# Kernel tuning notes

Hardware: AMD Instinct MI355X
Metric: run time of the kernel (lower is better)

Reference implementation:

```python
import jax, jax.numpy as jnp
import numpy as np

DIM = 1024
NUM_HEADS = 16
HEAD_DIM = DIM // NUM_HEADS
SCALE = HEAD_DIM ** -0.5


def setup_inputs() -> dict:
    key = jax.random.key(0)
    ks = jax.random.split(key, 6)
    B, N, C = 2, 2048, DIM
    std = C ** -0.5
    return {
        "x_t": jax.random.normal(ks[0], (B, N, C), dtype=jnp.float32),
        "x_s": jax.random.normal(ks[1], (B, N, C), dtype=jnp.float32),
        "W_q": jax.random.normal(ks[2], (C, C), dtype=jnp.float32) * std,
        "W_kv": jax.random.normal(ks[3], (C, 2 * C), dtype=jnp.float32) * std,
        "W_fuse": jax.random.normal(ks[4], (C, C), dtype=jnp.float32) * std,
        "b_fuse": jax.random.normal(ks[5], (C,), dtype=jnp.float32) * 0.01,
    }


def reference(x_t, x_s, W_q, W_kv, W_fuse, b_fuse):
    B, N, C = x_t.shape
    H, D = NUM_HEADS, HEAD_DIM
    # q projection (no bias, qkv_bias=False): [B,N,C] -> [B,H,N,D]
    q = (x_t @ W_q).reshape(B, N, H, D).transpose(0, 2, 1, 3)
    # kv projection: [B,N,2C] -> k,v each [B,H,N,D]
    kv = (x_s @ W_kv).reshape(B, N, 2, H, D).transpose(2, 0, 3, 1, 4)
    k, v = kv[0], kv[1]
    # attention scores [B,H,N,N]
    attn = jnp.einsum("bhnd,bhmd->bhnm", q, k) * SCALE
    attn = jax.nn.softmax(attn, axis=-1)
    # weighted values -> [B,N,C]
    a = jnp.einsum("bhnm,bhmd->bhnd", attn, v).transpose(0, 2, 1, 3).reshape(B, N, C)
    # fuse projection (with bias); dropouts are identity (p=0)
    return a @ W_fuse + b_fuse
```

## Files before the change

kernel.cpp:

```cpp
#include <hip/hip_runtime.h>

#define SEQ 2048

typedef short short8 __attribute__((ext_vector_type(8)));
typedef float floatx4 __attribute__((ext_vector_type(4)));

static __device__ __forceinline__ unsigned short f2bf(float f) {
    unsigned int u = __builtin_bit_cast(unsigned int, f);
    u = (u + 0x7fffu + ((u >> 16) & 1u)) >> 16;
    return (unsigned short)u;
}

#if __has_builtin(__builtin_amdgcn_cvt_pk_bf16_f32)
typedef __bf16 bf16x2 __attribute__((ext_vector_type(2)));
static __device__ __forceinline__ unsigned int pk_bf16(float a, float b) {
    bf16x2 v = __builtin_amdgcn_cvt_pk_bf16_f32(a, b);
    return __builtin_bit_cast(unsigned int, v);
}
#else
static __device__ __forceinline__ unsigned int pk_bf16(float a, float b) {
    return (unsigned int)f2bf(a) | ((unsigned int)f2bf(b) << 16);
}
#endif

#define GLD16(gp, lp)                                                        \
    __builtin_amdgcn_global_load_lds(                                        \
        (const __attribute__((address_space(1))) unsigned int*)(gp),         \
        (__attribute__((address_space(3))) unsigned int*)(lp), 16, 0, 0)

#define SWZ(row, col) ((col) ^ (((row) & 7) << 3))

__global__ void cvt2_kernel(const float4* __restrict__ a, const float4* __restrict__ b,
                            ushort4* __restrict__ oa, ushort4* __restrict__ ob, float sa) {
    int i = blockIdx.x * blockDim.x + threadIdx.x;
    if (i < 1048576) {
        float4 v = a[i];
        ushort4 o;
        o.x = f2bf(v.x * sa); o.y = f2bf(v.y * sa);
        o.z = f2bf(v.z * sa); o.w = f2bf(v.w * sa);
        oa[i] = o;
    } else {
        int j = i - 1048576;
        float4 v = b[j];
        ushort4 o;
        o.x = f2bf(v.x); o.y = f2bf(v.y);
        o.z = f2bf(v.z); o.w = f2bf(v.w);
        ob[j] = o;
    }
}

__global__ void transpose_all(const float* __restrict__ Wq, const float* __restrict__ Wkv,
                              const float* __restrict__ Wf,
                              unsigned short* __restrict__ oq, unsigned short* __restrict__ okv,
                              unsigned short* __restrict__ of_) {
    __shared__ float tile[32][33];
    int bx = blockIdx.x;
    const float* in; unsigned short* out; int N, t;
    if (bx < 1024)      { in = Wq;  out = oq;  N = 1024; t = bx; }
    else if (bx < 3072) { in = Wkv; out = okv; N = 2048; t = bx - 1024; }
    else                { in = Wf;  out = of_; N = 1024; t = bx - 3072; }
    int nb = N >> 5;
    int n0 = (t % nb) * 32, k0 = (t / nb) * 32;
    int tx = threadIdx.x, ty = threadIdx.y;
#pragma unroll
    for (int i = 0; i < 4; i++)
        tile[ty + i * 8][tx] = in[(size_t)(k0 + ty + i * 8) * N + n0 + tx];
    __syncthreads();
#pragma unroll
    for (int i = 0; i < 4; i++)
        out[(size_t)(n0 + ty + i * 8) * 1024 + k0 + tx] = f2bf(tile[tx][ty + i * 8]);
}

__global__ __launch_bounds__(256, 3)
void gemm_qkv(const unsigned short* __restrict__ xt,
              const unsigned short* __restrict__ xs,
              const unsigned short* __restrict__ wq,
              const unsigned short* __restrict__ wkv,
              unsigned short* __restrict__ q_ws,
              unsigned short* __restrict__ k_ws,
              unsigned short* __restrict__ vt_ws) {
    __shared__ unsigned short sA[128][64];
    __shared__ unsigned short sB[128][64];
    int tid = threadIdx.x, wave = tid >> 6, lane = tid & 63;
    int l15 = lane & 15, quad = lane >> 4;
    int cx = blockIdx.x;
    bool isq = cx < 8;
    const unsigned short* A  = isq ? xt : xs;
    const unsigned short* Bt = isq ? wq : wkv;
    int C0 = (isq ? cx : cx - 8) * 128;
    int R0 = blockIdx.y * 128;
    int wr = (wave >> 1) * 64, wc = (wave & 1) * 64;
    int srow = lane >> 3, scol = (lane & 7) * 8;

    floatx4 acc[4][4];
#pragma unroll
    for (int i = 0; i < 4; i++)
#pragma unroll
        for (int j = 0; j < 4; j++) acc[i][j] = (floatx4){0.f, 0.f, 0.f, 0.f};

    for (int kt = 0; kt < 16; kt++) {
        __syncthreads();
#pragma unroll
        for (int c = 0; c < 4; c++) {
            int rb = wave * 32 + c * 8;
            GLD16(&A [(size_t)(R0 + rb + srow) * 1024 + kt * 64 + scol], &sA[rb][0]);
            GLD16(&Bt[(size_t)(C0 + rb + srow) * 1024 + kt * 64 + scol], &sB[rb][0]);
        }
        __syncthreads();
#pragma unroll
        for (int ks = 0; ks < 2; ks++) {
            short8 af[4], bf[4];
#pragma unroll
            for (int mt = 0; mt < 4; mt++)
                af[mt] = *(const short8*)&sA[wr + mt * 16 + l15][ks * 32 + quad * 8];
#pragma unroll
            for (int nt = 0; nt < 4; nt++)
                bf[nt] = *(const short8*)&sB[wc + nt * 16 + l15][ks * 32 + quad * 8];
#pragma unroll
            for (int mt = 0; mt < 4; mt++)
#pragma unroll
                for (int nt = 0; nt < 4; nt++)
                    acc[mt][nt] = __builtin_amdgcn_mfma_f32_16x16x32_bf16(af[mt], bf[nt], acc[mt][nt], 0, 0, 0);
        }
    }

    int b = R0 >> 11, nb0 = (R0 & 2047) + wr;
#pragma unroll
    for (int mt = 0; mt < 4; mt++) {
#pragma unroll
        for (int nt = 0; nt < 4; nt++) {
            int col = C0 + wc + nt * 16 + l15;
            if (isq) {
                int h = col >> 6, d = col & 63;
#pragma unroll
                for (int r = 0; r < 4; r++) {
                    int n = nb0 + mt * 16 + quad * 4 + r;
                    q_ws[((size_t)((b * 16 + h) * 2048 + n)) * 64 + d] = f2bf(acc[mt][nt][r]);
                }
            } else if (col < 1024) {
                int h = col >> 6, d = col & 63;
#pragma unroll
                for (int r = 0; r < 4; r++) {
                    int n = nb0 + mt * 16 + quad * 4 + r;
                    k_ws[((size_t)((b * 16 + h) * 2048 + n)) * 64 + d] = f2bf(acc[mt][nt][r]);
                }
            } else {
                int cc = col - 1024, h = cc >> 6, d = cc & 63;
                int n = nb0 + mt * 16 + quad * 4;
                ushort4 pk;
                pk.x = f2bf(acc[mt][nt][0]); pk.y = f2bf(acc[mt][nt][1]);
                pk.z = f2bf(acc[mt][nt][2]); pk.w = f2bf(acc[mt][nt][3]);
                *(ushort4*)&vt_ws[((size_t)((b * 16 + h) * 64 + d)) * 2048 + n] = pk;
            }
        }
    }
}

__global__ __launch_bounds__(256, 3)
void gemm_fuse(const unsigned short* __restrict__ A,
               const unsigned short* __restrict__ Bt,
               float* __restrict__ out, const float* __restrict__ bias) {
    __shared__ unsigned short sA[128][64];
    __shared__ unsigned short sB[64][64];
    int tid = threadIdx.x, wave = tid >> 6, lane = tid & 63;
    int l15 = lane & 15, quad = lane >> 4;
    int R0 = blockIdx.y * 128, C0 = blockIdx.x * 64;
    int wr = (wave >> 1) * 64, wc = (wave & 1) * 32;
    int srow = lane >> 3, scol = (lane & 7) * 8;

    floatx4 acc[4][2];
#pragma unroll
    for (int i = 0; i < 4; i++)
#pragma unroll
        for (int j = 0; j < 2; j++) acc[i][j] = (floatx4){0.f, 0.f, 0.f, 0.f};

    for (int kt = 0; kt < 16; kt++) {
        __syncthreads();
#pragma unroll
        for (int c = 0; c < 4; c++) {
            int rb = wave * 32 + c * 8;
            GLD16(&A[(size_t)(R0 + rb + srow) * 1024 + kt * 64 + scol], &sA[rb][0]);
        }
#pragma unroll
        for (int c = 0; c < 2; c++) {
            int rb = wave * 16 + c * 8;
            GLD16(&Bt[(size_t)(C0 + rb + srow) * 1024 + kt * 64 + scol], &sB[rb][0]);
        }
        __syncthreads();
#pragma unroll
        for (int ks = 0; ks < 2; ks++) {
            short8 af[4], bf[2];
#pragma unroll
            for (int mt = 0; mt < 4; mt++)
                af[mt] = *(const short8*)&sA[wr + mt * 16 + l15][ks * 32 + quad * 8];
#pragma unroll
            for (int nt = 0; nt < 2; nt++)
                bf[nt] = *(const short8*)&sB[wc + nt * 16 + l15][ks * 32 + quad * 8];
#pragma unroll
            for (int mt = 0; mt < 4; mt++)
#pragma unroll
                for (int nt = 0; nt < 2; nt++)
                    acc[mt][nt] = __builtin_amdgcn_mfma_f32_16x16x32_bf16(af[mt], bf[nt], acc[mt][nt], 0, 0, 0);
        }
    }

#pragma unroll
    for (int mt = 0; mt < 4; mt++) {
#pragma unroll
        for (int r = 0; r < 4; r++) {
            int row = R0 + wr + mt * 16 + quad * 4 + r;
#pragma unroll
            for (int nt = 0; nt < 2; nt++) {
                int col = C0 + wc + nt * 16 + l15;
                out[(size_t)row * 1024 + col] = acc[mt][nt][r] + bias[col];
            }
        }
    }
}

__global__ __launch_bounds__(256, 4)
void attn_kernel(const unsigned short* __restrict__ Q,
                 const unsigned short* __restrict__ K,
                 const unsigned short* __restrict__ Vt,
                 unsigned short* __restrict__ Aout) {
    __shared__ unsigned short sQP[64][64];
    __shared__ unsigned short sK[2][64][64];
    __shared__ unsigned short sV[2][64][64];

    int tid = threadIdx.x, wave = tid >> 6, lane = tid & 63;
    int l15 = lane & 15, quad = lane >> 4;
    int bh = blockIdx.y, b = bh >> 4, h = bh & 15;
    int qr0 = blockIdx.x * 64;

    const unsigned short* Qp = Q + (size_t)bh * SEQ * 64;
    const unsigned short* Kp = K + (size_t)bh * SEQ * 64;
    const unsigned short* Vp = Vt + (size_t)bh * 64 * SEQ;

#pragma unroll
    for (int i = 0; i < 2; i++) {
        int ch = tid + i * 256;
        int row = ch >> 3, kc = (ch & 7) * 8;
        *(int4*)&sQP[row][SWZ(row, kc)] = *(const int4*)&Qp[(size_t)(qr0 + row) * 64 + kc];
        *(int4*)&sK[0][row][SWZ(row, kc)] = *(const int4*)&Kp[(size_t)row * 64 + kc];
        *(int4*)&sV[0][row][SWZ(row, kc)] = *(const int4*)&Vp[(size_t)row * SEQ + kc];
    }
    __syncthreads();

    short8 qf[2];
#pragma unroll
    for (int ks = 0; ks < 2; ks++) {
        int row = wave * 16 + l15;
        qf[ks] = *(const short8*)&sQP[row][SWZ(row, ks * 32 + quad * 8)];
    }
    __syncthreads();

    short8 vones;
#pragma unroll
    for (int i = 0; i < 8; i++) vones[i] = (short)0x3F80;

    floatx4 of[4];
#pragma unroll
    for (int i = 0; i < 4; i++) of[i] = (floatx4){0.f, 0.f, 0.f, 0.f};
    floatx4 of_l = (floatx4){0.f, 0.f, 0.f, 0.f};

    for (int kt = 0; kt < 32; kt++) {
        int p = kt & 1;
        int4 kreg[2], vreg[2];
        if (kt < 31) {
            int k0n = (kt + 1) * 64;
#pragma unroll
            for (int i = 0; i < 2; i++) {
                int ch = tid + i * 256;
                int row = ch >> 3, kc = (ch & 7) * 8;
                kreg[i] = *(const int4*)&Kp[(size_t)(k0n + row) * 64 + kc];
                vreg[i] = *(const int4*)&Vp[(size_t)row * SEQ + k0n + kc];
            }
        }

        floatx4 sacc[4];
        floatx4 zero = (floatx4){0.f, 0.f, 0.f, 0.f};
#pragma unroll
        for (int f = 0; f < 4; f++) {
            int krow = f * 16 + l15;
            short8 kf0 = *(const short8*)&sK[p][krow][SWZ(krow, quad * 8)];
            short8 kf1 = *(const short8*)&sK[p][krow][SWZ(krow, 32 + quad * 8)];
            floatx4 t = __builtin_amdgcn_mfma_f32_16x16x32_bf16(kf0, qf[0], zero, 0, 0, 0);
            sacc[f] = __builtin_amdgcn_mfma_f32_16x16x32_bf16(kf1, qf[1], t, 0, 0, 0);
        }

        {
            int prow = wave * 16 + l15;
#pragma unroll
            for (int f = 0; f < 4; f++) {
                float p0 = __builtin_amdgcn_exp2f(sacc[f][0]);
                float p1 = __builtin_amdgcn_exp2f(sacc[f][1]);
                float p2 = __builtin_amdgcn_exp2f(sacc[f][2]);
                float p3 = __builtin_amdgcn_exp2f(sacc[f][3]);
                uint2 pk;
                pk.x = pk_bf16(p0, p1);
                pk.y = pk_bf16(p2, p3);
                *(uint2*)&sQP[prow][SWZ(prow, f * 16 + quad * 4)] = pk;
            }
        }
        asm volatile("s_waitcnt lgkmcnt(0)" ::: "memory");

#pragma unroll
        for (int s2 = 0; s2 < 2; s2++) {
            int prow = wave * 16 + l15;
            short8 pf = *(const short8*)&sQP[prow][SWZ(prow, s2 * 32 + quad * 8)];
#pragma unroll
            for (int dt = 0; dt < 4; dt++) {
                int vrow = dt * 16 + l15;
                short8 vf = *(const short8*)&sV[p][vrow][SWZ(vrow, s2 * 32 + quad * 8)];
                of[dt] = __builtin_amdgcn_mfma_f32_16x16x32_bf16(vf, pf, of[dt], 0, 0, 0);
            }
            of_l = __builtin_amdgcn_mfma_f32_16x16x32_bf16(vones, pf, of_l, 0, 0, 0);
        }

        if (kt < 31) {
#pragma unroll
            for (int i = 0; i < 2; i++) {
                int ch = tid + i * 256;
                int row = ch >> 3, kc = (ch & 7) * 8;
                *(int4*)&sK[p ^ 1][row][SWZ(row, kc)] = kreg[i];
                *(int4*)&sV[p ^ 1][row][SWZ(row, kc)] = vreg[i];
            }
            __syncthreads();
        }
    }

    {
        float inv = 1.f / of_l[0];
        int row = qr0 + wave * 16 + l15;
        size_t base = (size_t)(b * SEQ + row) * 1024 + h * 64;
#pragma unroll
        for (int dt = 0; dt < 4; dt++) {
            uint2 o;
            o.x = pk_bf16(of[dt][0] * inv, of[dt][1] * inv);
            o.y = pk_bf16(of[dt][2] * inv, of[dt][3] * inv);
            *(uint2*)&Aout[base + dt * 16 + quad * 4] = o;
        }
    }
}

extern "C" void kernel_launch(void* const* d_in, const int* in_sizes, int n_in,
                              void* d_out, int out_size, void* d_ws, size_t ws_size,
                              hipStream_t stream) {
    const float* x_t  = (const float*)d_in[0];
    const float* x_s  = (const float*)d_in[1];
    const float* W_q  = (const float*)d_in[2];
    const float* W_kv = (const float*)d_in[3];
    const float* W_f  = (const float*)d_in[4];
    const float* b_f  = (const float*)d_in[5];
    float* out = (float*)d_out;

    char* ws = (char*)d_ws;
    const size_t MB = 1u << 20;
    unsigned short* xt_bf = (unsigned short*)(ws);
    unsigned short* xs_bf = (unsigned short*)(ws + 8 * MB);
    unsigned short* wq_t  = (unsigned short*)(ws + 16 * MB);
    unsigned short* wkv_t = (unsigned short*)(ws + 18 * MB);
    unsigned short* wf_t  = (unsigned short*)(ws + 22 * MB);
    unsigned short* q_ws  = (unsigned short*)(ws + 24 * MB);
    unsigned short* k_ws  = (unsigned short*)(ws + 32 * MB);
    unsigned short* vt_ws = (unsigned short*)(ws + 40 * MB);
    unsigned short* a_ws  = (unsigned short*)(ws + 48 * MB);

    cvt2_kernel<<<8192, 256, 0, stream>>>((const float4*)x_t, (const float4*)x_s,
                                          (ushort4*)xt_bf, (ushort4*)xs_bf,
                                          0.125f * 1.44269504088896340736f);
    transpose_all<<<4096, dim3(32, 8), 0, stream>>>(W_q, W_kv, W_f, wq_t, wkv_t, wf_t);

    gemm_qkv<<<dim3(24, 32), 256, 0, stream>>>(xt_bf, xs_bf, wq_t, wkv_t, q_ws, k_ws, vt_ws);
    attn_kernel<<<dim3(32, 32), 256, 0, stream>>>(q_ws, k_ws, vt_ws, a_ws);
    gemm_fuse<<<dim3(16, 32), 256, 0, stream>>>(a_ws, wf_t, out, b_f);
}
```

Measured before the change: 209.6 us.

## Split keys across waves in attention with LDS DMA loads and fp16 PV

The attention kernel is restructured so each wave owns a 16-key slice of every 64-key tile and computes all 64 query rows, instead of each wave owning 16 query rows. P stays in registers as fp16 and feeds 16x16x16 f16 MFMAs directly, and V is written as pre-swizzled fp16 by the projection kernel. K/V tiles are loaded with global_load_lds DMA, and K is stored pre-swizzled so it can be read without an LDS staging round-trip. The cost is a cross-wave reduction of outputs and row sums through LDS at the end, more accumulator registers (occupancy hint lowered to 2), and fp16 range/precision for V and P.

```diff
diff --git a/kernel.cpp b/kernel.cpp
--- a/kernel.cpp
+++ b/kernel.cpp
@@ -4,6 +4,9 @@
 
 typedef short short8 __attribute__((ext_vector_type(8)));
 typedef float floatx4 __attribute__((ext_vector_type(4)));
+typedef unsigned short ushort4v __attribute__((ext_vector_type(4)));
+typedef unsigned int uint2v __attribute__((ext_vector_type(2)));
+typedef __fp16 f16x4 __attribute__((ext_vector_type(4)));
 
 static __device__ __forceinline__ unsigned short f2bf(float f) {
     unsigned int u = __builtin_bit_cast(unsigned int, f);
@@ -23,12 +26,15 @@
 }
 #endif
 
+static __device__ __forceinline__ unsigned int pk_f16(float a, float b) {
+    auto v = __builtin_amdgcn_cvt_pkrtz(a, b);
+    return __builtin_bit_cast(unsigned int, v);
+}
+
 #define GLD16(gp, lp)                                                        \
     __builtin_amdgcn_global_load_lds(                                        \
         (const __attribute__((address_space(1))) unsigned int*)(gp),         \
         (__attribute__((address_space(3))) unsigned int*)(lp), 16, 0, 0)
-
-#define SWZ(row, col) ((col) ^ (((row) & 7) << 3))
 
 __global__ void cvt2_kernel(const float4* __restrict__ a, const float4* __restrict__ b,
                             ushort4* __restrict__ oa, ushort4* __restrict__ ob, float sa) {
@@ -142,15 +148,16 @@
 #pragma unroll
                 for (int r = 0; r < 4; r++) {
                     int n = nb0 + mt * 16 + quad * 4 + r;
-                    k_ws[((size_t)((b * 16 + h) * 2048 + n)) * 64 + d] = f2bf(acc[mt][nt][r]);
+                    k_ws[((size_t)((b * 16 + h) * 2048 + n)) * 64 + (d ^ ((n & 7) << 3))] = f2bf(acc[mt][nt][r]);
                 }
             } else {
                 int cc = col - 1024, h = cc >> 6, d = cc & 63;
-                int n = nb0 + mt * 16 + quad * 4;
-                ushort4 pk;
-                pk.x = f2bf(acc[mt][nt][0]); pk.y = f2bf(acc[mt][nt][1]);
-                pk.z = f2bf(acc[mt][nt][2]); pk.w = f2bf(acc[mt][nt][3]);
-                *(ushort4*)&vt_ws[((size_t)((b * 16 + h) * 64 + d)) * 2048 + n] = pk;
+                int n0 = nb0 + mt * 16 + quad * 4;
+                int coln = (n0 & ~63) | ((n0 & 63) ^ ((d & 7) << 3));
+                uint2v pk;
+                pk.x = pk_f16(acc[mt][nt][0], acc[mt][nt][1]);
+                pk.y = pk_f16(acc[mt][nt][2], acc[mt][nt][3]);
+                *(uint2v*)&vt_ws[((size_t)((b * 16 + h) * 64 + d)) * 2048 + coln] = pk;
             }
         }
     }
@@ -218,14 +225,13 @@
     }
 }
 
-__global__ __launch_bounds__(256, 4)
+__global__ __launch_bounds__(256, 2)
 void attn_kernel(const unsigned short* __restrict__ Q,
                  const unsigned short* __restrict__ K,
                  const unsigned short* __restrict__ Vt,
                  unsigned short* __restrict__ Aout) {
-    __shared__ unsigned short sQP[64][64];
-    __shared__ unsigned short sK[2][64][64];
-    __shared__ unsigned short sV[2][64][64];
+    __shared__ __align__(16) unsigned short smem[16384];
+    __shared__ float lred[4][4][16];
 
     int tid = threadIdx.x, wave = tid >> 6, lane = tid & 63;
     int l15 = lane & 15, quad = lane >> 4;
@@ -236,111 +242,132 @@
     const unsigned short* Kp = K + (size_t)bh * SEQ * 64;
     const unsigned short* Vp = Vt + (size_t)bh * 64 * SEQ;
 
-#pragma unroll
-    for (int i = 0; i < 2; i++) {
-        int ch = tid + i * 256;
-        int row = ch >> 3, kc = (ch & 7) * 8;
-        *(int4*)&sQP[row][SWZ(row, kc)] = *(const int4*)&Qp[(size_t)(qr0 + row) * 64 + kc];
-        *(int4*)&sK[0][row][SWZ(row, kc)] = *(const int4*)&Kp[(size_t)row * 64 + kc];
-        *(int4*)&sV[0][row][SWZ(row, kc)] = *(const int4*)&Vp[(size_t)row * SEQ + kc];
-    }
+    int srow = lane >> 3, scol = (lane & 7) * 8;
+    int wk0 = wave * 16;
+
+#pragma unroll
+    for (int j = 0; j < 2; j++) {
+        int rb = wk0 + j * 8;
+        GLD16(&Kp[(size_t)(rb + srow) * 64 + scol], &smem[rb * 64]);
+        GLD16(&Vp[(size_t)(rb + srow) * 2048 + scol], &smem[8192 + rb * 64]);
+    }
+
+    short8 qf[4][2];
+#pragma unroll
+    for (int nt = 0; nt < 4; nt++)
+#pragma unroll
+        for (int ks = 0; ks < 2; ks++)
+            qf[nt][ks] = *(const short8*)&Qp[(size_t)(qr0 + nt * 16 + l15) * 64 + ks * 32 + quad * 8];
+
+    floatx4 of[4][4];
+#pragma unroll
+    for (int i = 0; i < 4; i++)
+#pragma unroll
+        for (int j = 0; j < 4; j++) of[i][j] = (floatx4){0.f, 0.f, 0.f, 0.f};
+    float lsum[4] = {0.f, 0.f, 0.f, 0.f};
+
     __syncthreads();
 
-    short8 qf[2];
-#pragma unroll
-    for (int ks = 0; ks < 2; ks++) {
-        int row = wave * 16 + l15;
-        qf[ks] = *(const short8*)&sQP[row][SWZ(row, ks * 32 + quad * 8)];
-    }
-    __syncthreads();
-
-    short8 vones;
-#pragma unroll
-    for (int i = 0; i < 8; i++) vones[i] = (short)0x3F80;
-
-    floatx4 of[4];
-#pragma unroll
-    for (int i = 0; i < 4; i++) of[i] = (floatx4){0.f, 0.f, 0.f, 0.f};
-    floatx4 of_l = (floatx4){0.f, 0.f, 0.f, 0.f};
-
+    int krow = wk0 + l15;
+    int ksw = (l15 & 7) << 3;
+    int kaddr0 = krow * 64 + ((quad * 8) ^ ksw);
+    int kaddr1 = krow * 64 + ((32 + quad * 8) ^ ksw);
+    int vcol = (wk0 + quad * 4) ^ ksw;
+
+#pragma unroll 2
     for (int kt = 0; kt < 32; kt++) {
-        int p = kt & 1;
-        int4 kreg[2], vreg[2];
+        int p = kt & 1, pb = p * 4096;
         if (kt < 31) {
             int k0n = (kt + 1) * 64;
 #pragma unroll
-            for (int i = 0; i < 2; i++) {
-                int ch = tid + i * 256;
-                int row = ch >> 3, kc = (ch & 7) * 8;
-                kreg[i] = *(const int4*)&Kp[(size_t)(k0n + row) * 64 + kc];
-                vreg[i] = *(const int4*)&Vp[(size_t)row * SEQ + k0n + kc];
+            for (int j = 0; j < 2; j++) {
+                int rb = wk0 + j * 8;
+                GLD16(&Kp[(size_t)(k0n + rb + srow) * 64 + scol], &smem[(pb ^ 4096) + rb * 64]);
+                GLD16(&Vp[(size_t)(rb + srow) * 2048 + k0n + scol], &smem[8192 + (pb ^ 4096) + rb * 64]);
             }
         }
 
-        floatx4 sacc[4];
-        floatx4 zero = (floatx4){0.f, 0.f, 0.f, 0.f};
-#pragma unroll
-        for (int f = 0; f < 4; f++) {
-            int krow = f * 16 + l15;
-            short8 kf0 = *(const short8*)&sK[p][krow][SWZ(krow, quad * 8)];
-            short8 kf1 = *(const short8*)&sK[p][krow][SWZ(krow, 32 + quad * 8)];
-            floatx4 t = __builtin_amdgcn_mfma_f32_16x16x32_bf16(kf0, qf[0], zero, 0, 0, 0);
-            sacc[f] = __builtin_amdgcn_mfma_f32_16x16x32_bf16(kf1, qf[1], t, 0, 0, 0);
-        }
-
-        {
-            int prow = wave * 16 + l15;
-#pragma unroll
-            for (int f = 0; f < 4; f++) {
-                float p0 = __builtin_amdgcn_exp2f(sacc[f][0]);
-                float p1 = __builtin_amdgcn_exp2f(sacc[f][1]);
-                float p2 = __builtin_amdgcn_exp2f(sacc[f][2]);
-                float p3 = __builtin_amdgcn_exp2f(sacc[f][3]);
-                uint2 pk;
-                pk.x = pk_bf16(p0, p1);
-                pk.y = pk_bf16(p2, p3);
-                *(uint2*)&sQP[prow][SWZ(prow, f * 16 + quad * 4)] = pk;
-            }
-        }
-        asm volatile("s_waitcnt lgkmcnt(0)" ::: "memory");
-
-#pragma unroll
-        for (int s2 = 0; s2 < 2; s2++) {
-            int prow = wave * 16 + l15;
-            short8 pf = *(const short8*)&sQP[prow][SWZ(prow, s2 * 32 + quad * 8)];
-#pragma unroll
-            for (int dt = 0; dt < 4; dt++) {
-                int vrow = dt * 16 + l15;
-                short8 vf = *(const short8*)&sV[p][vrow][SWZ(vrow, s2 * 32 + quad * 8)];
-                of[dt] = __builtin_amdgcn_mfma_f32_16x16x32_bf16(vf, pf, of[dt], 0, 0, 0);
-            }
-            of_l = __builtin_amdgcn_mfma_f32_16x16x32_bf16(vones, pf, of_l, 0, 0, 0);
-        }
-
-        if (kt < 31) {
-#pragma unroll
-            for (int i = 0; i < 2; i++) {
-                int ch = tid + i * 256;
-                int row = ch >> 3, kc = (ch & 7) * 8;
-                *(int4*)&sK[p ^ 1][row][SWZ(row, kc)] = kreg[i];
-                *(int4*)&sV[p ^ 1][row][SWZ(row, kc)] = vreg[i];
-            }
-            __syncthreads();
-        }
-    }
-
-    {
-        float inv = 1.f / of_l[0];
-        int row = qr0 + wave * 16 + l15;
-        size_t base = (size_t)(b * SEQ + row) * 1024 + h * 64;
+        short8 kf0 = *(const short8*)&smem[pb + kaddr0];
+        short8 kf1 = *(const short8*)&smem[pb + kaddr1];
+        f16x4 pf[4];
+#pragma unroll
+        for (int nt = 0; nt < 4; nt++) {
+            floatx4 zero = (floatx4){0.f, 0.f, 0.f, 0.f};
+            floatx4 s = __builtin_amdgcn_mfma_f32_16x16x32_bf16(kf0, qf[nt][0], zero, 0, 0, 0);
+            s = __builtin_amdgcn_mfma_f32_16x16x32_bf16(kf1, qf[nt][1], s, 0, 0, 0);
+            float p0 = __builtin_amdgcn_exp2f(s[0]);
+            float p1 = __builtin_amdgcn_exp2f(s[1]);
+            float p2 = __builtin_amdgcn_exp2f(s[2]);
+            float p3 = __builtin_amdgcn_exp2f(s[3]);
+            lsum[nt] += (p0 + p1) + (p2 + p3);
+            uint2v u;
+            u.x = pk_f16(p0, p1);
+            u.y = pk_f16(p2, p3);
+            pf[nt] = __builtin_bit_cast(f16x4, u);
+        }
+
 #pragma unroll
         for (int dt = 0; dt < 4; dt++) {
-            uint2 o;
-            o.x = pk_bf16(of[dt][0] * inv, of[dt][1] * inv);
-            o.y = pk_bf16(of[dt][2] * inv, of[dt][3] * inv);
-            *(uint2*)&Aout[base + dt * 16 + quad * 4] = o;
-        }
-    }
+            int vrow = dt * 16 + l15;
+            ushort4v vv = *(const ushort4v*)&smem[8192 + pb + vrow * 64 + vcol];
+            f16x4 vf = __builtin_bit_cast(f16x4, vv);
+#pragma unroll
+            for (int nt = 0; nt < 4; nt++)
+                of[dt][nt] = __builtin_amdgcn_mfma_f32_16x16x16f16(vf, pf[nt], of[dt][nt], 0, 0, 0);
+        }
+        __syncthreads();
+    }
+
+#pragma unroll
+    for (int nt = 0; nt < 4; nt++) {
+        float l = lsum[nt];
+        l += __shfl_xor(l, 16, 64);
+        l += __shfl_xor(l, 32, 64);
+        lsum[nt] = l;
+    }
+    if (quad == 0) {
+#pragma unroll
+        for (int nt = 0; nt < 4; nt++) lred[wave][nt][l15] = lsum[nt];
+    }
+
+    float* red = (float*)smem;
+
+#define RED_WRITE(C, DTC)                                                          \
+    _Pragma("unroll")                                                              \
+    for (int nt = 0; nt < 4; nt++)                                                 \
+        *(floatx4*)&red[((C) * 4 + wave) * 1024 + nt * 256 + lane * 4] = of[DTC][nt];
+
+#define RED_STORE(DT, C, W0, W1, W2)                                               \
+    {                                                                              \
+        size_t obase = (size_t)(b * SEQ + qr0) * 1024 + h * 64 + (DT) * 16 + quad * 4; \
+        _Pragma("unroll")                                                          \
+        for (int nt = 0; nt < 4; nt++) {                                           \
+            floatx4 a0 = *(const floatx4*)&red[((C) * 4 + (W0)) * 1024 + nt * 256 + lane * 4]; \
+            floatx4 a1 = *(const floatx4*)&red[((C) * 4 + (W1)) * 1024 + nt * 256 + lane * 4]; \
+            floatx4 a2 = *(const floatx4*)&red[((C) * 4 + (W2)) * 1024 + nt * 256 + lane * 4]; \
+            floatx4 s = of[DT][nt] + a0 + a1 + a2;                                 \
+            float lt = lred[0][nt][l15] + lred[1][nt][l15] + lred[2][nt][l15] + lred[3][nt][l15]; \
+            float inv = 1.f / lt;                                                  \
+            uint2v o;                                                              \
+            o.x = pk_bf16(s[0] * inv, s[1] * inv);                                 \
+            o.y = pk_bf16(s[2] * inv, s[3] * inv);                                 \
+            *(uint2v*)&Aout[obase + (size_t)(nt * 16 + l15) * 1024] = o;           \
+        }                                                                          \
+    }
+
+    RED_WRITE(0, 0)
+    RED_WRITE(1, 1)
+    __syncthreads();
+    if (wave == 0)      RED_STORE(0, 0, 1, 2, 3)
+    else if (wave == 1) RED_STORE(1, 1, 0, 2, 3)
+    __syncthreads();
+    RED_WRITE(0, 2)
+    RED_WRITE(1, 3)
+    __syncthreads();
+    if (wave == 2)      RED_STORE(2, 0, 0, 1, 3)
+    else if (wave == 3) RED_STORE(3, 1, 0, 1, 2)
+#undef RED_WRITE
+#undef RED_STORE
 }
 
 extern "C" void kernel_launch(void* const* d_in, const int* in_sizes, int n_in,
```

Measured after the change: 214.4 us. 1.02x slower.
